# Performance work log

Hardware: AMD Instinct MI355X
Metric: run time of the kernel (lower is better)

## Reference

```python
import jax, jax.numpy as jnp
import numpy as np

G, S, M = 4, 2048, 1024   # groups (batch), tokens per group, emb dim
E, H, K = 8, 4096, 2      # experts, mlp dim, top-k
CAP = int(K * S / E * 1.25)  # expert capacity = 640
AUX_COEF, Z_COEF = 0.01, 0.001


def setup_inputs() -> dict:
    key = jax.random.key(0)
    k1, k2, k3, k4, k5 = jax.random.split(key, 5)
    return {
        "inputs": jax.random.normal(k1, (G, S, M), jnp.float32),
        "paddings": jnp.zeros((G, S), jnp.float32),  # 1.0 = padded token
        "router_w": jax.random.normal(k2, (M, E), jnp.float32) / np.sqrt(M),
        "wi_gate": jax.random.normal(k3, (E, M, H), jnp.float32) / np.sqrt(M),
        "wi_0": jax.random.normal(k4, (E, M, H), jnp.float32) / np.sqrt(M),
        "wo": jax.random.normal(k5, (E, H, M), jnp.float32) / np.sqrt(H),
    }


def reference(inputs, paddings, router_w, wi_gate, wi_0, wo):
    # Router
    logits = jnp.einsum('gsm,me->gse', inputs, router_w)          # [G,S,E]
    probs = jax.nn.softmax(logits, axis=-1)
    top_p, top_i = jax.lax.top_k(probs, K)                        # [G,S,K]

    nonpad = 1.0 - paddings                                       # [G,S]
    exp_mask = jax.nn.one_hot(top_i, E, dtype=jnp.float32)        # [G,S,K,E]
    exp_mask = exp_mask * nonpad[:, :, None, None]

    # Position in expert (capacity-limited), priority by token order then k slot
    mask_flat = exp_mask.reshape(G, S * K, E)
    pos = jnp.cumsum(mask_flat, axis=1) * mask_flat               # 1-indexed where assigned
    keep = mask_flat * (pos <= CAP)
    pos_oh = jax.nn.one_hot((pos - 1.0).astype(jnp.int32), CAP, dtype=jnp.float32)  # [G,SK,E,CAP]
    dispatch_k = (keep[..., None] * pos_oh).reshape(G, S, K, E, CAP)
    dispatch = dispatch_k.sum(axis=2)                             # [G,S,E,CAP]
    combine = jnp.einsum('gsk,gskec->gsec', top_p, dispatch_k)    # [G,S,E,CAP]

    # Dispatch -> gated expert FFN -> combine
    expert_in = jnp.einsum('gsec,gsm->egcm', dispatch, inputs)    # [E,G,CAP,M]
    h = jax.nn.silu(jnp.einsum('egcm,emh->egch', expert_in, wi_gate)) \
        * jnp.einsum('egcm,emh->egch', expert_in, wi_0)           # [E,G,CAP,H]
    expert_out = jnp.einsum('egch,ehm->egcm', h, wo)              # [E,G,CAP,M]
    output = jnp.einsum('gsec,egcm->gsm', combine, expert_out)    # [G,S,M]

    # Aux losses: load-balancing (Switch style) + router z-loss
    em = jnp.max(jax.nn.one_hot(top_i, E, dtype=jnp.float32), axis=-2)       # [G,S,E]
    lb = jnp.mean(jnp.mean(em, axis=-2) * jnp.mean(probs, axis=-2)) * E * E
    z = jnp.mean(jax.nn.logsumexp(logits, axis=-1) ** 2)
    aux_loss = AUX_COEF * lb + Z_COEF * z
    return output, aux_loss
```

## Files before the change

kernel.cpp:

```cpp
#include <hip/hip_runtime.h>
#include <hip/hip_bf16.h>
#include <math.h>

#define G 4
#define S 2048
#define MDIM 1024
#define E 8
#define HDIM 4096
#define TOPK 2
#define CAP 640
#define GC (G*CAP)

typedef __attribute__((ext_vector_type(8))) short bf16x8;
typedef __attribute__((ext_vector_type(4))) short s16x4;
typedef __attribute__((ext_vector_type(4))) float f32x4;
typedef __attribute__((ext_vector_type(16))) float f32x16;
typedef unsigned int u32;
typedef unsigned short u16;

#define MFMA32(a,b,c) __builtin_amdgcn_mfma_f32_32x32x16_bf16(a,b,c,0,0,0)
#define BAR() __builtin_amdgcn_s_barrier()

__device__ __forceinline__ u16 f2bf(float f) {
    union { float f; u32 u; } v; v.f = f;
    u32 r = v.u + 0x7fffu + ((v.u >> 16) & 1u);
    return (u16)(r >> 16);
}

__device__ __forceinline__ void gload16(const char* gp, char* lp) {
    __builtin_amdgcn_global_load_lds((const __attribute__((address_space(1))) u32*)gp,
                                     (__attribute__((address_space(3))) u32*)lp,
                                     16, 0, 0);
}

__device__ __forceinline__ int swz128(int r) { return ((r >> 1) & 7) << 4; }

__global__ __launch_bounds__(256) void transpose_cvt(const float* __restrict__ in,
                                                     u16* __restrict__ out, int R, int C) {
    int e = blockIdx.z;
    const float* ine = in + (size_t)e * R * C;
    u16* oute = out + (size_t)e * R * C;
    __shared__ float tile[64][68];
    int t = threadIdx.x;
    int x0 = blockIdx.x * 64, y0 = blockIdx.y * 64;
    int lx = (t & 15) * 4, ly = t >> 4;
    #pragma unroll
    for (int i = 0; i < 4; ++i) {
        f32x4 v = *(const f32x4*)(ine + (size_t)(y0 + ly + i * 16) * C + x0 + lx);
        *(f32x4*)&tile[ly + i * 16][lx] = v;
    }
    __syncthreads();
    int rr0 = (t & 15) * 4, cb = t >> 4;
    #pragma unroll
    for (int p = 0; p < 4; ++p) {
        int cc = cb + p * 16;
        s16x4 pk;
        #pragma unroll
        for (int j = 0; j < 4; ++j) pk[j] = (short)f2bf(tile[rr0 + j][cc]);
        *(s16x4*)(oute + (size_t)(x0 + cc) * R + y0 + rr0) = pk;
    }
}

__global__ __launch_bounds__(256) void router_kernel(const float* __restrict__ inp,
                                                     const float* __restrict__ rw,
                                                     int* __restrict__ top_i,
                                                     float* __restrict__ top_p,
                                                     float* __restrict__ partials) {
    int wid = threadIdx.x >> 6, lane = threadIdx.x & 63;
    int tok = blockIdx.x * 4 + wid;
    const float* x = inp + (size_t)tok * MDIM;
    float acc[E] = {0.f,0.f,0.f,0.f,0.f,0.f,0.f,0.f};
    #pragma unroll
    for (int rep = 0; rep < 4; ++rep) {
        int m0 = rep * 256 + lane * 4;
        f32x4 xv = *(const f32x4*)(x + m0);
        #pragma unroll
        for (int j = 0; j < 4; ++j) {
            const float* r = rw + (size_t)(m0 + j) * E;
            float xj = xv[j];
            #pragma unroll
            for (int e = 0; e < E; ++e) acc[e] += xj * r[e];
        }
    }
    #pragma unroll
    for (int e = 0; e < E; ++e)
        #pragma unroll
        for (int off = 32; off; off >>= 1) acc[e] += __shfl_down(acc[e], off);

    __shared__ float part[4][17];
    if (lane == 0) {
        float mx = acc[0];
        #pragma unroll
        for (int e = 1; e < E; ++e) mx = fmaxf(mx, acc[e]);
        float p[E], sum = 0.f;
        #pragma unroll
        for (int e = 0; e < E; ++e) { p[e] = expf(acc[e] - mx); sum += p[e]; }
        float inv = 1.f / sum;
        #pragma unroll
        for (int e = 0; e < E; ++e) p[e] *= inv;
        float lse = logf(sum) + mx;
        int i0 = 0;
        #pragma unroll
        for (int e = 1; e < E; ++e) if (acc[e] > acc[i0]) i0 = e;
        int i1 = (i0 == 0) ? 1 : 0;
        #pragma unroll
        for (int e = 0; e < E; ++e) if (e != i0 && acc[e] > acc[i1]) i1 = e;
        top_i[tok*2+0] = i0; top_i[tok*2+1] = i1;
        top_p[tok*2+0] = p[i0]; top_p[tok*2+1] = p[i1];
        #pragma unroll
        for (int e = 0; e < E; ++e) { part[wid][e] = p[e]; part[wid][8+e] = 0.f; }
        part[wid][8+i0] = 1.f; part[wid][8+i1] = 1.f;
        part[wid][16] = lse * lse;
    }
    __syncthreads();
    if (threadIdx.x < 17) {
        float v = part[0][threadIdx.x] + part[1][threadIdx.x] +
                  part[2][threadIdx.x] + part[3][threadIdx.x];
        partials[(size_t)blockIdx.x * 17 + threadIdx.x] = v;
    }
}

__global__ __launch_bounds__(256) void reduce_partials(const float* __restrict__ partials,
                                                       float* __restrict__ sums) {
    int g = blockIdx.x, t = threadIdx.x;
    float loc[17];
    #pragma unroll
    for (int c = 0; c < 17; ++c) loc[c] = 0.f;
    for (int r = t; r < 1024; r += 256) {
        const float* pr = partials + ((size_t)g * 1024 + r) * 17;
        #pragma unroll
        for (int c = 0; c < 17; ++c) loc[c] += pr[c];
    }
    __shared__ float red[256];
    for (int c = 0; c < 17; ++c) {
        red[t] = loc[c]; __syncthreads();
        for (int off = 128; off; off >>= 1) {
            if (t < off) red[t] += red[t + off];
            __syncthreads();
        }
        if (t == 0) sums[g * 17 + c] = red[0];
        __syncthreads();
    }
}

__global__ void aux_final(const float* __restrict__ sums, float* __restrict__ out) {
    float lb = 0.f, z = 0.f;
    for (int g = 0; g < G; ++g) {
        for (int e = 0; e < E; ++e)
            lb += (sums[g*17 + 8 + e] / (float)S) * (sums[g*17 + e] / (float)S);
        z += sums[g*17 + 16];
    }
    lb = lb / (float)(G * E) * (float)(E * E);
    z /= (float)(G * S);
    out[(size_t)G * S * MDIM] = 0.01f * lb + 0.001f * z;
}

__global__ __launch_bounds__(256) void scan_kernel(const int* __restrict__ top_i,
                                                   const float* __restrict__ pad,
                                                   int* __restrict__ slot_token,
                                                   int* __restrict__ token_c) {
    int b = blockIdx.x; int g = b >> 3, e = b & 7;
    int t = threadIdx.x;
    __shared__ int sums[256];
    int base = t * 16;
    int run = 0; unsigned mask16 = 0; int loc[16];
    #pragma unroll
    for (int j = 0; j < 16; ++j) {
        int i = base + j; int s = i >> 1, k = i & 1;
        int ex = top_i[((size_t)(g * S + s)) * 2 + k];
        int m = (ex == e) && (pad[g * S + s] == 0.f);
        run += m; loc[j] = run; mask16 |= ((unsigned)m << j);
    }
    sums[t] = run; __syncthreads();
    for (int off = 1; off < 256; off <<= 1) {
        int v = (t >= off) ? sums[t - off] : 0;
        __syncthreads();
        sums[t] += v;
        __syncthreads();
    }
    int excl = sums[t] - run;
    #pragma unroll
    for (int j = 0; j < 16; ++j) {
        if ((mask16 >> j) & 1u) {
            int pos = excl + loc[j];
            if (pos <= CAP) {
                int i = base + j; int s = i >> 1, k = i & 1;
                slot_token[((size_t)(e * G + g)) * CAP + (pos - 1)] = s;
                token_c[((size_t)(g * S + s)) * 2 + k] = pos - 1;
            }
        }
    }
}

__global__ __launch_bounds__(128) void gather_kernel(const float* __restrict__ inp,
                                                     const int* __restrict__ slot_token,
                                                     u16* __restrict__ X) {
    int row = blockIdx.x;
    int t = threadIdx.x;
    int s = slot_token[row];
    int g = (row % GC) / CAP;
    bf16x8 v;
    if (s >= 0) {
        const float* src = inp + ((size_t)(g * S + s)) * MDIM + t * 8;
        f32x4 a = *(const f32x4*)src;
        f32x4 b = *(const f32x4*)(src + 4);
        #pragma unroll
        for (int j = 0; j < 4; ++j) { v[j] = (short)f2bf(a[j]); v[4+j] = (short)f2bf(b[j]); }
    } else {
        #pragma unroll
        for (int j = 0; j < 8; ++j) v[j] = 0;
    }
    *(bf16x8*)(X + (size_t)row * MDIM + t * 8) = v;
}

__global__ __launch_bounds__(512, 1) void gemm_ffn12_v9(
        const u16* __restrict__ Xb, const u16* __restrict__ WgT,
        const u16* __restrict__ W0T, u16* __restrict__ Hb) {
    extern __shared__ char smem[];
    const int NK = MDIM / 64;
    int bid = blockIdx.x;
    int swz = (bid & 7) * 320 + (bid >> 3);
    int mt = swz % 10, nt = (swz / 10) & 31, e = swz / 320;
    const char* A  = (const char*)(Xb  + (size_t)e * GC * MDIM   + (size_t)mt * 256 * MDIM);
    const char* Bg = (const char*)(WgT + (size_t)e * HDIM * MDIM + (size_t)nt * 128 * MDIM);
    const char* B0 = (const char*)(W0T + (size_t)e * HDIM * MDIM + (size_t)nt * 128 * MDIM);
    int tid = threadIdx.x, w = tid >> 6, l = tid & 63;
    int wm = w >> 2, wn = w & 3;
    int lr = l & 31, lk = l >> 5;
    int lswz = ((lr >> 1) & 7) << 4;

    int koff[4];
    #pragma unroll
    for (int ks = 0; ks < 4; ++ks) koff[ks] = (ks * 32 + lk * 16) ^ lswz;
    int baseA[4];
    #pragma unroll
    for (int rb = 0; rb < 4; ++rb) baseA[rb] = (wm * 128 + rb * 32 + lr) * 128;
    int baseB = (wn * 32 + lr) * 128;

    const char* srcA[4]; const char* srcG[2]; const char* srcO[2];
    #pragma unroll
    for (int p = 0; p < 4; ++p) {
        int gr = p * 64 + w * 8 + (l >> 3);
        srcA[p] = A + (size_t)gr * (MDIM * 2) + (((l & 7) * 16) ^ swz128(gr));
    }
    #pragma unroll
    for (int p = 0; p < 2; ++p) {
        int gr = p * 64 + w * 8 + (l >> 3);
        srcG[p] = Bg + (size_t)gr * (MDIM * 2) + (((l & 7) * 16) ^ swz128(gr));
        srcO[p] = B0 + (size_t)gr * (MDIM * 2) + (((l & 7) * 16) ^ swz128(gr));
    }

    f32x16 zz;
    #pragma unroll
    for (int i = 0; i < 16; ++i) zz[i] = 0.f;
    f32x16 ag[4], ao[4];
    #pragma unroll
    for (int rb = 0; rb < 4; ++rb) { ag[rb] = zz; ao[rb] = zz; }

    auto stage = [&](int tt) {
        int kk = tt * 128;
        char* dst = smem + (tt & 1) * 65536;
        #pragma unroll
        for (int p = 0; p < 4; ++p)
            gload16(srcA[p] + kk, dst + (p * 64 + w * 8) * 128);
        #pragma unroll
        for (int p = 0; p < 2; ++p) {
            gload16(srcG[p] + kk, dst + 32768 + (p * 64 + w * 8) * 128);
            gload16(srcO[p] + kk, dst + 49152 + (p * 64 + w * 8) * 128);
        }
    };

    stage(0);
    asm volatile("s_waitcnt vmcnt(0)" ::: "memory");
    BAR();

    #pragma unroll 1
    for (int t = 0; t < NK; ++t) {
        if (t + 1 < NK) stage(t + 1);
        const char* bufc = smem + (t & 1) * 65536;
        #pragma unroll
        for (int ks = 0; ks < 4; ++ks) {
            bf16x8 bg = *(const bf16x8*)(bufc + 32768 + baseB + koff[ks]);
            bf16x8 bo = *(const bf16x8*)(bufc + 49152 + baseB + koff[ks]);
            bf16x8 af[4];
            #pragma unroll
            for (int rb = 0; rb < 4; ++rb)
                af[rb] = *(const bf16x8*)(bufc + baseA[rb] + koff[ks]);
            __builtin_amdgcn_s_setprio(1);
            #pragma unroll
            for (int rb = 0; rb < 4; ++rb) {
                ag[rb] = MFMA32(bg, af[rb], ag[rb]);
                ao[rb] = MFMA32(bo, af[rb], ao[rb]);
            }
            __builtin_amdgcn_s_setprio(0);
        }
        asm volatile("s_waitcnt vmcnt(0)" ::: "memory");
        BAR();
    }

    u16* He = Hb + (size_t)e * GC * HDIM;
    int row0 = mt * 256 + wm * 128 + lr;
    int col0 = nt * 128 + wn * 32 + lk * 4;
    #pragma unroll
    for (int rb = 0; rb < 4; ++rb) {
        size_t rowoff = (size_t)(row0 + rb * 32) * HDIM;
        #pragma unroll
        for (int q = 0; q < 4; ++q) {
            s16x4 pk;
            #pragma unroll
            for (int r = 0; r < 4; ++r) {
                float gv = ag[rb][q * 4 + r], ov = ao[rb][q * 4 + r];
                float hv = gv / (1.f + __expf(-gv)) * ov;
                pk[r] = (short)f2bf(hv);
            }
            *(s16x4*)(He + rowoff + col0 + q * 8) = pk;
        }
    }
}

__global__ __launch_bounds__(512, 1) void gemm_out_v9(
        const u16* __restrict__ Hb, const u16* __restrict__ WoT,
        float* __restrict__ EO) {
    extern __shared__ char smem[];
    const int NK = HDIM / 64;
    int bid = blockIdx.x;
    int swz = (bid & 7) * 80 + (bid >> 3);
    int nt = swz & 3, mt = (swz / 4) % 20, e = swz / 80;
    const char* A = (const char*)(Hb  + (size_t)e * GC * HDIM   + (size_t)mt * 128 * HDIM);
    const char* B = (const char*)(WoT + (size_t)e * MDIM * HDIM + (size_t)nt * 256 * HDIM);
    int tid = threadIdx.x, w = tid >> 6, l = tid & 63;
    int wm = w >> 2, wn = w & 3;
    int lr = l & 31, lk = l >> 5;
    int lswz = ((lr >> 1) & 7) << 4;

    int koff[4];
    #pragma unroll
    for (int ks = 0; ks < 4; ++ks) koff[ks] = (ks * 32 + lk * 16) ^ lswz;
    int baseA[2], baseB[2];
    #pragma unroll
    for (int rb = 0; rb < 2; ++rb) baseA[rb] = (wm * 64 + rb * 32 + lr) * 128;
    #pragma unroll
    for (int cb = 0; cb < 2; ++cb) baseB[cb] = (wn * 64 + cb * 32 + lr) * 128;

    const char* srcA[2]; const char* srcB[4];
    #pragma unroll
    for (int p = 0; p < 2; ++p) {
        int gr = p * 64 + w * 8 + (l >> 3);
        srcA[p] = A + (size_t)gr * (HDIM * 2) + (((l & 7) * 16) ^ swz128(gr));
    }
    #pragma unroll
    for (int p = 0; p < 4; ++p) {
        int gr = p * 64 + w * 8 + (l >> 3);
        srcB[p] = B + (size_t)gr * (HDIM * 2) + (((l & 7) * 16) ^ swz128(gr));
    }

    f32x16 zz;
    #pragma unroll
    for (int i = 0; i < 16; ++i) zz[i] = 0.f;
    f32x16 acc[2][2];
    #pragma unroll
    for (int i = 0; i < 2; ++i)
        #pragma unroll
        for (int j = 0; j < 2; ++j) acc[i][j] = zz;

    auto stage = [&](int tt) {
        int kk = tt * 128;
        char* dst = smem + (tt & 1) * 49152;
        #pragma unroll
        for (int p = 0; p < 2; ++p)
            gload16(srcA[p] + kk, dst + (p * 64 + w * 8) * 128);
        #pragma unroll
        for (int p = 0; p < 4; ++p)
            gload16(srcB[p] + kk, dst + 16384 + (p * 64 + w * 8) * 128);
    };

    stage(0);
    asm volatile("s_waitcnt vmcnt(0)" ::: "memory");
    BAR();

    #pragma unroll 1
    for (int t = 0; t < NK; ++t) {
        if (t + 1 < NK) stage(t + 1);
        const char* bufc = smem + (t & 1) * 49152;
        #pragma unroll
        for (int ks = 0; ks < 4; ++ks) {
            bf16x8 bf[2], af[2];
            #pragma unroll
            for (int cb = 0; cb < 2; ++cb)
                bf[cb] = *(const bf16x8*)(bufc + 16384 + baseB[cb] + koff[ks]);
            #pragma unroll
            for (int rb = 0; rb < 2; ++rb)
                af[rb] = *(const bf16x8*)(bufc + baseA[rb] + koff[ks]);
            __builtin_amdgcn_s_setprio(1);
            #pragma unroll
            for (int rb = 0; rb < 2; ++rb)
                #pragma unroll
                for (int cb = 0; cb < 2; ++cb)
                    acc[rb][cb] = MFMA32(bf[cb], af[rb], acc[rb][cb]);
            __builtin_amdgcn_s_setprio(0);
        }
        asm volatile("s_waitcnt vmcnt(0)" ::: "memory");
        BAR();
    }

    float* Ee = EO + (size_t)e * GC * MDIM;
    int row0 = mt * 128 + wm * 64 + lr;
    int col0 = nt * 256 + wn * 64 + lk * 4;
    #pragma unroll
    for (int rb = 0; rb < 2; ++rb) {
        size_t rowoff = (size_t)(row0 + rb * 32) * MDIM;
        #pragma unroll
        for (int cb = 0; cb < 2; ++cb)
            #pragma unroll
            for (int q = 0; q < 4; ++q) {
                f32x4 v;
                #pragma unroll
                for (int r = 0; r < 4; ++r) v[r] = acc[rb][cb][q * 4 + r];
                *(f32x4*)(Ee + rowoff + col0 + cb * 32 + q * 8) = v;
            }
    }
}

__global__ __launch_bounds__(256) void combine_kernel(const float* __restrict__ EO,
                                                      const int* __restrict__ top_i,
                                                      const float* __restrict__ top_p,
                                                      const int* __restrict__ token_c,
                                                      float* __restrict__ out) {
    int tok = blockIdx.x, t = threadIdx.x;
    int g = tok >> 11;
    f32x4 acc = {0.f, 0.f, 0.f, 0.f};
    #pragma unroll
    for (int k = 0; k < 2; ++k) {
        int c = token_c[tok * 2 + k];
        if (c >= 0) {
            int e = top_i[tok * 2 + k];
            float p = top_p[tok * 2 + k];
            const float* src = EO + ((size_t)e * GC + g * CAP + c) * MDIM + t * 4;
            f32x4 v = *(const f32x4*)src;
            #pragma unroll
            for (int j = 0; j < 4; ++j) acc[j] += p * v[j];
        }
    }
    *(f32x4*)(out + (size_t)tok * MDIM + t * 4) = acc;
}

extern "C" void kernel_launch(void* const* d_in, const int* in_sizes, int n_in,
                              void* d_out, int out_size, void* d_ws, size_t ws_size,
                              hipStream_t stream) {
    (void)in_sizes; (void)n_in; (void)out_size; (void)ws_size;
    const float* inputs   = (const float*)d_in[0];
    const float* paddings = (const float*)d_in[1];
    const float* router_w = (const float*)d_in[2];
    const float* wi_gate  = (const float*)d_in[3];
    const float* wi_0     = (const float*)d_in[4];
    const float* wo       = (const float*)d_in[5];
    float* out = (float*)d_out;

    char* p = (char*)d_ws;
    u16* WgT = (u16*)p; p += (size_t)E * HDIM * MDIM * 2;
    u16* W0T = (u16*)p; p += (size_t)E * HDIM * MDIM * 2;
    u16* WoT = (u16*)p; p += (size_t)E * HDIM * MDIM * 2;
    u16* Xb  = (u16*)p; p += (size_t)E * GC * MDIM * 2;
    u16* Hb  = (u16*)p; p += (size_t)E * GC * HDIM * 2;
    float* EO = (float*)p; p += (size_t)E * GC * MDIM * 4;
    int*   top_i = (int*)p;   p += (size_t)G * S * TOPK * 4;
    float* top_p = (float*)p; p += (size_t)G * S * TOPK * 4;
    int*   token_c = (int*)p; p += (size_t)G * S * TOPK * 4;
    int*   slot_token = (int*)p; p += (size_t)E * G * CAP * 4;
    float* partials = (float*)p; p += (size_t)4096 * 17 * 4;
    float* sums = (float*)p; p += 4 * 17 * 4;

    hipMemsetAsync(token_c, 0xFF, (size_t)G * S * TOPK * 4, stream);
    hipMemsetAsync(slot_token, 0xFF, (size_t)E * G * CAP * 4, stream);

    hipFuncSetAttribute((const void*)gemm_ffn12_v9,
                        hipFuncAttributeMaxDynamicSharedMemorySize, 131072);
    hipFuncSetAttribute((const void*)gemm_out_v9,
                        hipFuncAttributeMaxDynamicSharedMemorySize, 98304);

    transpose_cvt<<<dim3(HDIM/64, MDIM/64, E), 256, 0, stream>>>(wi_gate, WgT, MDIM, HDIM);
    transpose_cvt<<<dim3(HDIM/64, MDIM/64, E), 256, 0, stream>>>(wi_0,   W0T, MDIM, HDIM);
    transpose_cvt<<<dim3(MDIM/64, HDIM/64, E), 256, 0, stream>>>(wo,     WoT, HDIM, MDIM);

    router_kernel<<<G * S / 4, 256, 0, stream>>>(inputs, router_w, top_i, top_p, partials);
    reduce_partials<<<G, 256, 0, stream>>>(partials, sums);
    scan_kernel<<<G * E, 256, 0, stream>>>(top_i, paddings, slot_token, token_c);
    gather_kernel<<<E * GC, 128, 0, stream>>>(inputs, slot_token, Xb);
    gemm_ffn12_v9<<<2560, 512, 131072, stream>>>(Xb, WgT, W0T, Hb);
    gemm_out_v9<<<640, 512, 98304, stream>>>(Hb, WoT, EO);
    combine_kernel<<<G * S, 256, 0, stream>>>(EO, top_i, top_p, token_c, out);
    aux_final<<<1, 1, 0, stream>>>(sums, out);
}
```

Baseline: 787.7 us.

## Merge small prep, scan/reduce and combine/aux kernels into fewer launches

Merges the three weight transpose-convert launches with the router into one prep kernel that splits work by block index. Reduce-partials is folded into the scan kernel and the aux-loss finalisation into the combine kernel. This cuts launch count and the gaps between small dependent kernels, so the transposes and the router can run concurrently. The cost is a larger static LDS footprint per block in the prep kernel, which may lower occupancy for the router blocks.

Measured after the change: 763.2 us. 1.03x faster.

```diff
diff --git a/kernel.cpp b/kernel.cpp
--- a/kernel.cpp
+++ b/kernel.cpp
@@ -10,6 +10,7 @@
 #define TOPK 2
 #define CAP 640
 #define GC (G*CAP)
+#define RBLK (G*S/4)
 
 typedef __attribute__((ext_vector_type(8))) short bf16x8;
 typedef __attribute__((ext_vector_type(4))) short s16x4;
@@ -35,14 +36,14 @@
 
 __device__ __forceinline__ int swz128(int r) { return ((r >> 1) & 7) << 4; }
 
-__global__ __launch_bounds__(256) void transpose_cvt(const float* __restrict__ in,
-                                                     u16* __restrict__ out, int R, int C) {
-    int e = blockIdx.z;
+__device__ void transpose_body(const float* __restrict__ in, u16* __restrict__ out,
+                               int R, int C, int tb, float (*tile)[68]) {
+    int nbx = C / 64, nby = R / 64;
+    int bx = tb % nbx, by = (tb / nbx) % nby, e = tb / (nbx * nby);
     const float* ine = in + (size_t)e * R * C;
     u16* oute = out + (size_t)e * R * C;
-    __shared__ float tile[64][68];
     int t = threadIdx.x;
-    int x0 = blockIdx.x * 64, y0 = blockIdx.y * 64;
+    int x0 = bx * 64, y0 = by * 64;
     int lx = (t & 15) * 4, ly = t >> 4;
     #pragma unroll
     for (int i = 0; i < 4; ++i) {
@@ -61,13 +62,25 @@
     }
 }
 
-__global__ __launch_bounds__(256) void router_kernel(const float* __restrict__ inp,
-                                                     const float* __restrict__ rw,
-                                                     int* __restrict__ top_i,
-                                                     float* __restrict__ top_p,
-                                                     float* __restrict__ partials) {
+__global__ __launch_bounds__(256) void prep_kernel(
+        const float* __restrict__ inp, const float* __restrict__ rw,
+        const float* __restrict__ wi_gate, const float* __restrict__ wi_0,
+        const float* __restrict__ wo,
+        u16* __restrict__ WgT, u16* __restrict__ W0T, u16* __restrict__ WoT,
+        int* __restrict__ top_i, float* __restrict__ top_p,
+        float* __restrict__ partials) {
+    __shared__ float tile[64][68];
+    __shared__ float part[4][17];
+    int bid = blockIdx.x;
+    if (bid >= RBLK) {
+        int tb = bid - RBLK;
+        if (tb < 8192)       transpose_body(wi_gate, WgT, MDIM, HDIM, tb, tile);
+        else if (tb < 16384) transpose_body(wi_0,   W0T, MDIM, HDIM, tb - 8192, tile);
+        else                 transpose_body(wo,     WoT, HDIM, MDIM, tb - 16384, tile);
+        return;
+    }
     int wid = threadIdx.x >> 6, lane = threadIdx.x & 63;
-    int tok = blockIdx.x * 4 + wid;
+    int tok = bid * 4 + wid;
     const float* x = inp + (size_t)tok * MDIM;
     float acc[E] = {0.f,0.f,0.f,0.f,0.f,0.f,0.f,0.f};
     #pragma unroll
@@ -87,7 +100,6 @@
         #pragma unroll
         for (int off = 32; off; off >>= 1) acc[e] += __shfl_down(acc[e], off);
 
-    __shared__ float part[4][17];
     if (lane == 0) {
         float mx = acc[0];
         #pragma unroll
@@ -116,52 +128,41 @@
     if (threadIdx.x < 17) {
         float v = part[0][threadIdx.x] + part[1][threadIdx.x] +
                   part[2][threadIdx.x] + part[3][threadIdx.x];
-        partials[(size_t)blockIdx.x * 17 + threadIdx.x] = v;
-    }
-}
-
-__global__ __launch_bounds__(256) void reduce_partials(const float* __restrict__ partials,
-                                                       float* __restrict__ sums) {
-    int g = blockIdx.x, t = threadIdx.x;
-    float loc[17];
-    #pragma unroll
-    for (int c = 0; c < 17; ++c) loc[c] = 0.f;
-    for (int r = t; r < 1024; r += 256) {
-        const float* pr = partials + ((size_t)g * 1024 + r) * 17;
-        #pragma unroll
-        for (int c = 0; c < 17; ++c) loc[c] += pr[c];
-    }
+        partials[(size_t)bid * 17 + threadIdx.x] = v;
+    }
+}
+
+__global__ __launch_bounds__(256) void scan_reduce_kernel(
+        const int* __restrict__ top_i, const float* __restrict__ pad,
+        const float* __restrict__ partials,
+        int* __restrict__ slot_token, int* __restrict__ token_c,
+        float* __restrict__ sums_out) {
+    __shared__ int sums[256];
     __shared__ float red[256];
-    for (int c = 0; c < 17; ++c) {
-        red[t] = loc[c]; __syncthreads();
-        for (int off = 128; off; off >>= 1) {
-            if (t < off) red[t] += red[t + off];
+    int bid = blockIdx.x;
+    int t = threadIdx.x;
+    if (bid >= 32) {
+        int g = bid - 32;
+        float loc[17];
+        #pragma unroll
+        for (int c = 0; c < 17; ++c) loc[c] = 0.f;
+        for (int r = t; r < 512; r += 256) {
+            const float* pr = partials + ((size_t)g * 512 + r) * 17;
+            #pragma unroll
+            for (int c = 0; c < 17; ++c) loc[c] += pr[c];
+        }
+        for (int c = 0; c < 17; ++c) {
+            red[t] = loc[c]; __syncthreads();
+            for (int off = 128; off; off >>= 1) {
+                if (t < off) red[t] += red[t + off];
+                __syncthreads();
+            }
+            if (t == 0) sums_out[g * 17 + c] = red[0];
             __syncthreads();
         }
-        if (t == 0) sums[g * 17 + c] = red[0];
-        __syncthreads();
-    }
-}
-
-__global__ void aux_final(const float* __restrict__ sums, float* __restrict__ out) {
-    float lb = 0.f, z = 0.f;
-    for (int g = 0; g < G; ++g) {
-        for (int e = 0; e < E; ++e)
-            lb += (sums[g*17 + 8 + e] / (float)S) * (sums[g*17 + e] / (float)S);
-        z += sums[g*17 + 16];
-    }
-    lb = lb / (float)(G * E) * (float)(E * E);
-    z /= (float)(G * S);
-    out[(size_t)G * S * MDIM] = 0.01f * lb + 0.001f * z;
-}
-
-__global__ __launch_bounds__(256) void scan_kernel(const int* __restrict__ top_i,
-                                                   const float* __restrict__ pad,
-                                                   int* __restrict__ slot_token,
-                                                   int* __restrict__ token_c) {
-    int b = blockIdx.x; int g = b >> 3, e = b & 7;
-    int t = threadIdx.x;
-    __shared__ int sums[256];
+        return;
+    }
+    int g = bid >> 3, e = bid & 7;
     int base = t * 16;
     int run = 0; unsigned mask16 = 0; int loc[16];
     #pragma unroll
@@ -421,12 +422,26 @@
     }
 }
 
-__global__ __launch_bounds__(256) void combine_kernel(const float* __restrict__ EO,
-                                                      const int* __restrict__ top_i,
-                                                      const float* __restrict__ top_p,
-                                                      const int* __restrict__ token_c,
-                                                      float* __restrict__ out) {
-    int tok = blockIdx.x, t = threadIdx.x;
+__global__ __launch_bounds__(256) void combine_aux_kernel(
+        const float* __restrict__ EO, const int* __restrict__ top_i,
+        const float* __restrict__ top_p, const int* __restrict__ token_c,
+        const float* __restrict__ sums, float* __restrict__ out) {
+    int bid = blockIdx.x;
+    if (bid == G * S) {
+        if (threadIdx.x == 0) {
+            float lb = 0.f, z = 0.f;
+            for (int g = 0; g < G; ++g) {
+                for (int e = 0; e < E; ++e)
+                    lb += (sums[g*17 + 8 + e] / (float)S) * (sums[g*17 + e] / (float)S);
+                z += sums[g*17 + 16];
+            }
+            lb = lb / (float)(G * E) * (float)(E * E);
+            z /= (float)(G * S);
+            out[(size_t)G * S * MDIM] = 0.01f * lb + 0.001f * z;
+        }
+        return;
+    }
+    int tok = bid, t = threadIdx.x;
     int g = tok >> 11;
     f32x4 acc = {0.f, 0.f, 0.f, 0.f};
     #pragma unroll
@@ -467,7 +482,7 @@
     float* top_p = (float*)p; p += (size_t)G * S * TOPK * 4;
     int*   token_c = (int*)p; p += (size_t)G * S * TOPK * 4;
     int*   slot_token = (int*)p; p += (size_t)E * G * CAP * 4;
-    float* partials = (float*)p; p += (size_t)4096 * 17 * 4;
+    float* partials = (float*)p; p += (size_t)RBLK * 17 * 4;
     float* sums = (float*)p; p += 4 * 17 * 4;
 
     hipMemsetAsync(token_c, 0xFF, (size_t)G * S * TOPK * 4, stream);
@@ -478,16 +493,13 @@
     hipFuncSetAttribute((const void*)gemm_out_v9,
                         hipFuncAttributeMaxDynamicSharedMemorySize, 98304);
 
-    transpose_cvt<<<dim3(HDIM/64, MDIM/64, E), 256, 0, stream>>>(wi_gate, WgT, MDIM, HDIM);
-    transpose_cvt<<<dim3(HDIM/64, MDIM/64, E), 256, 0, stream>>>(wi_0,   W0T, MDIM, HDIM);
-    transpose_cvt<<<dim3(MDIM/64, HDIM/64, E), 256, 0, stream>>>(wo,     WoT, HDIM, MDIM);
-
-    router_kernel<<<G * S / 4, 256, 0, stream>>>(inputs, router_w, top_i, top_p, partials);
-    reduce_partials<<<G, 256, 0, stream>>>(partials, sums);
-    scan_kernel<<<G * E, 256, 0, stream>>>(top_i, paddings, slot_token, token_c);
+    prep_kernel<<<RBLK + 24576, 256, 0, stream>>>(inputs, router_w, wi_gate, wi_0, wo,
+                                                  WgT, W0T, WoT, top_i, top_p, partials);
+    scan_reduce_kernel<<<36, 256, 0, stream>>>(top_i, paddings, partials,
+                                               slot_token, token_c, sums);
     gather_kernel<<<E * GC, 128, 0, stream>>>(inputs, slot_token, Xb);
     gemm_ffn12_v9<<<2560, 512, 131072, stream>>>(Xb, WgT, W0T, Hb);
     gemm_out_v9<<<640, 512, 98304, stream>>>(Hb, WoT, EO);
-    combine_kernel<<<G * S, 256, 0, stream>>>(EO, top_i, top_p, token_c, out);
-    aux_final<<<1, 1, 0, stream>>>(sums, out);
-}
+    combine_aux_kernel<<<G * S + 1, 256, 0, stream>>>(EO, top_i, top_p, token_c,
+                                                      sums, out);
+}
```
